# Performance work log

Measured on AMD Instinct MI355X. Metric: run time of the kernel, lower is better.

Reference implementation:

```python
import jax, jax.numpy as jnp
import numpy as np

NUM_COLORS = 10
COLOR_MAPPING_W = 0.4
CONSISTENCY_W = 0.3
RULE_W = 0.2
EXACT_BONUS = 5.0


def _color_rules(targets, num_colors):
    # Vectorized equivalent of per-batch torch.unique(): sorted unique colors
    # of each grid written into the first slots of a [B, 10] rules tensor.
    B = targets.shape[0]
    colors = jnp.arange(num_colors)
    presence = jnp.any(targets[:, :, :, None] == colors, axis=(1, 2))  # [B, 10]
    pos = jnp.cumsum(presence.astype(jnp.int32), axis=1) - 1           # slot index per color
    cols = jnp.where(presence, pos, num_colors)                        # absent -> dump slot
    rules = jnp.zeros((B, num_colors + 1), dtype=jnp.float32)
    rules = rules.at[jnp.arange(B)[:, None], cols].set(
        colors.astype(jnp.float32) * presence.astype(jnp.float32))
    return rules[:, :num_colors]


def setup_inputs() -> dict:
    key = jax.random.key(0)
    k1, k2, k3, k4 = jax.random.split(key, 4)
    B, C, H, W = 4096, NUM_COLORS, 30, 30
    return {
        "color_output": jax.random.normal(k1, (B, C, H, W), dtype=jnp.float32),
        "targets": jax.random.randint(k2, (B, H, W), 0, C),
        "color_attention": jax.random.uniform(k3, (B, H, W, C), dtype=jnp.float32),
        "lstm_rules": jax.random.normal(k4, (B, C), dtype=jnp.float32),
    }


def reference(color_output, targets, color_attention, lstm_rules):
    B, C, H, W = color_output.shape
    # exact-match cross entropy (mean over B*H*W)
    logp = jax.nn.log_softmax(color_output, axis=1)               # [B,C,H,W]
    ce = -jnp.take_along_axis(logp, targets[:, None], axis=1).mean()
    pred_colors = jnp.argmax(color_output, axis=1)                # [B,H,W]
    eq = (pred_colors == targets).astype(jnp.float32)
    exact_count = eq.sum()
    # color mapping: MSE(attention, one_hot(targets))
    onehot = jax.nn.one_hot(targets, C, dtype=jnp.float32)        # [B,H,W,C]
    color_mapping = jnp.mean((color_attention - onehot) ** 2)
    # sliding 2x2 window consistency, fused: avg over windows of (1 - mean eq)
    s = eq[:, :-1, :-1] + eq[:, 1:, :-1] + eq[:, :-1, 1:] + eq[:, 1:, 1:]
    consistency = 1.0 - s.mean() / 4.0
    # rule learning: MSE against per-batch sorted-unique-color rules
    rule_target = _color_rules(targets, C)
    rule_loss = jnp.mean((lstm_rules - rule_target) ** 2)
    total = (ce + COLOR_MAPPING_W * color_mapping
             + CONSISTENCY_W * consistency + RULE_W * rule_loss)
    total = total - (exact_count / B) * EXACT_BONUS  # bonus is 0 when count is 0
    total = jnp.maximum(total, 0.001)
    return (total, ce, color_mapping, consistency, rule_loss, exact_count)
```

## Files before the change

kernel.cpp:

```cpp
#include <hip/hip_runtime.h>


namespace {
constexpr int kB = 4096;
constexpr int kC = 10;
constexpr int kH = 30;
constexpr int kW = 30;
constexpr int kHW = kH * kW;
constexpr int kCHW = kC * kHW;
constexpr int kQuadsPerB = kHW / 4;
constexpr int kQuads = kB * kQuadsPerB;
constexpr int kAttF4 = kB * kCHW / 4;
constexpr int kGrid = 2048;
constexpr int kThreads = 256;
constexpr int kStride = kGrid * kThreads;
}

__global__ __launch_bounds__(kThreads) void iris_att_sq(
    const float* __restrict__ att_g, float* __restrict__ cmsq_part) {
    const int tid = threadIdx.x;
    float sq = 0.f;
    for (int idx = blockIdx.x * kThreads + tid; idx < kAttF4; idx += kStride) {
        const float4 v = reinterpret_cast<const float4*>(att_g)[idx];
        sq += v.x * v.x + v.y * v.y + v.z * v.z + v.w * v.w;
    }
#pragma unroll
    for (int off = 32; off > 0; off >>= 1) sq += __shfl_down(sq, off);
    __shared__ float s[4];
    if ((tid & 63) == 0) s[tid >> 6] = sq;
    __syncthreads();
    if (tid == 0) cmsq_part[blockIdx.x] = s[0] + s[1] + s[2] + s[3];
}

__global__ __launch_bounds__(kThreads) void iris_ce(
    const float* __restrict__ logits_g,
    const int* __restrict__ targets_g,
    const float* __restrict__ att_g,
    float* __restrict__ ce_part,
    float* __restrict__ cmat_part,
    unsigned* __restrict__ weq_part,
    unsigned* __restrict__ eq_part)
{
    const int tid = threadIdx.x;
    float ce_acc = 0.f, at_acc = 0.f;
    unsigned weq_acc = 0u, eq_acc = 0u;

    for (int q = blockIdx.x * kThreads + tid; q < kQuads; q += kStride) {
        const int b = q / kQuadsPerB;
        const int i = q - b * kQuadsPerB;
        const int p0 = 4 * i;

        const int4 tv = *reinterpret_cast<const int4*>(targets_g + (size_t)b * kHW + p0);
        const int ta[4] = {tv.x, tv.y, tv.z, tv.w};

        const float* __restrict__ ap = att_g + (size_t)b * kCHW + (size_t)p0 * kC;
        at_acc += ap[0 * kC + ta[0]] + ap[1 * kC + ta[1]] +
                  ap[2 * kC + ta[2]] + ap[3 * kC + ta[3]];

        const float* __restrict__ lg = logits_g + (size_t)b * kCHW + p0;
        float m[4], s[4], xt[4];
        int am[4];
#pragma unroll
        for (int j = 0; j < 4; ++j) { m[j] = -3.4e38f; s[j] = 0.f; xt[j] = 0.f; am[j] = 0; }
#pragma unroll
        for (int c = 0; c < kC; ++c) {
            const float4 v = *reinterpret_cast<const float4*>(lg + c * kHW);
            const float xv[4] = {v.x, v.y, v.z, v.w};
#pragma unroll
            for (int j = 0; j < 4; ++j) {
                const bool gt = xv[j] > m[j];
                const float mn = gt ? xv[j] : m[j];
                s[j] = s[j] * __expf(m[j] - mn) + __expf(xv[j] - mn);
                m[j] = mn;
                am[j] = gt ? c : am[j];
                xt[j] = (c == ta[j]) ? xv[j] : xt[j];
            }
        }
#pragma unroll
        for (int j = 0; j < 4; ++j) {
            ce_acc += m[j] + __logf(s[j]) - xt[j];
            const unsigned eq = (am[j] == ta[j]) ? 1u : 0u;
            eq_acc += eq;
            const int p = p0 + j;
            const int h = p / kW;
            const int w = p - h * kW;
            weq_acc += eq * (((h == 0 || h == kH - 1) ? 1u : 2u) *
                             ((w == 0 || w == kW - 1) ? 1u : 2u));
        }
    }

#pragma unroll
    for (int off = 32; off > 0; off >>= 1) {
        ce_acc  += __shfl_down(ce_acc, off);
        at_acc  += __shfl_down(at_acc, off);
        weq_acc += __shfl_down(weq_acc, off);
        eq_acc  += __shfl_down(eq_acc, off);
    }
    __shared__ float sf[2][4];
    __shared__ unsigned su[2][4];
    const int wave = tid >> 6;
    if ((tid & 63) == 0) {
        sf[0][wave] = ce_acc; sf[1][wave] = at_acc;
        su[0][wave] = weq_acc; su[1][wave] = eq_acc;
    }
    __syncthreads();
    if (tid == 0) {
        ce_part[blockIdx.x]   = sf[0][0] + sf[0][1] + sf[0][2] + sf[0][3];
        cmat_part[blockIdx.x] = sf[1][0] + sf[1][1] + sf[1][2] + sf[1][3];
        weq_part[blockIdx.x]  = su[0][0] + su[0][1] + su[0][2] + su[0][3];
        eq_part[blockIdx.x]   = su[1][0] + su[1][1] + su[1][2] + su[1][3];
    }
}

__global__ __launch_bounds__(64) void iris_rules(
    const int* __restrict__ targets_g, const float* __restrict__ rules_g,
    float* __restrict__ rule_part) {
    const int b = blockIdx.x;
    const int lane = threadIdx.x;
    const int* __restrict__ tgt = targets_g + (size_t)b * kHW;
    unsigned mask = 0u;
    for (int k = lane; k < kHW; k += 64) mask |= 1u << tgt[k];
#pragma unroll
    for (int off = 32; off > 0; off >>= 1) mask |= __shfl_down(mask, off);
    if (lane == 0) {
        const float* __restrict__ lr = rules_g + (size_t)b * kC;
        unsigned mrem = mask;
        float rl = 0.f;
#pragma unroll
        for (int s2 = 0; s2 < kC; ++s2) {
            float v = 0.f;
            if (mrem) {
                v = (float)(__ffs(mrem) - 1);
                mrem &= mrem - 1u;
            }
            const float d = lr[s2] - v;
            rl += d * d;
        }
        rule_part[b] = rl;
    }
}

__global__ __launch_bounds__(1024) void iris_finalize(
    const float* __restrict__ ce_part,
    const float* __restrict__ cmat_part,
    const float* __restrict__ cmsq_part,
    const unsigned* __restrict__ weq_part,
    const unsigned* __restrict__ eq_part,
    const float* __restrict__ rule_part,
    float* __restrict__ out) {
    const int tid = threadIdx.x;
    double ce = 0.0, cma = 0.0, cms = 0.0, rl = 0.0;
    unsigned long long weq = 0ull, eqc = 0ull;
#pragma unroll
    for (int k = 0; k < 2; ++k) {
        const int i = tid + 1024 * k;
        ce  += (double)ce_part[i];
        cma += (double)cmat_part[i];
        cms += (double)cmsq_part[i];
        weq += (unsigned long long)weq_part[i];
        eqc += (unsigned long long)eq_part[i];
    }
#pragma unroll
    for (int k = 0; k < 4; ++k) rl += (double)rule_part[tid + 1024 * k];
#pragma unroll
    for (int off = 32; off > 0; off >>= 1) {
        ce  += __shfl_down(ce, off);
        cma += __shfl_down(cma, off);
        cms += __shfl_down(cms, off);
        rl  += __shfl_down(rl, off);
        weq += __shfl_down(weq, off);
        eqc += __shfl_down(eqc, off);
    }
    __shared__ double sd[4][16];
    __shared__ unsigned long long su[2][16];
    const int wave = tid >> 6;
    if ((tid & 63) == 0) {
        sd[0][wave] = ce; sd[1][wave] = cma; sd[2][wave] = cms; sd[3][wave] = rl;
        su[0][wave] = weq; su[1][wave] = eqc;
    }
    __syncthreads();
    if (tid == 0) {
        ce = 0.0; cma = 0.0; cms = 0.0; rl = 0.0; weq = 0ull; eqc = 0ull;
#pragma unroll
        for (int i = 0; i < 16; ++i) {
            ce += sd[0][i]; cma += sd[1][i]; cms += sd[2][i]; rl += sd[3][i];
            weq += su[0][i]; eqc += su[1][i];
        }
        const double npix = (double)kB * kHW;
        const double ce_m = ce / npix;
        const double cm_m = (cms - 2.0 * cma + npix) / (npix * kC);
        const double s_mean = (double)weq / ((double)kB * (kH - 1) * (kW - 1));
        const double cons = 1.0 - s_mean / 4.0;
        const double rl_m = rl / ((double)kB * kC);
        const double exact = (double)eqc;
        double total = ce_m + 0.4 * cm_m + 0.3 * cons + 0.2 * rl_m
                       - (exact / (double)kB) * 5.0;
        if (total < 0.001) total = 0.001;
        out[0] = (float)total;
        out[1] = (float)ce_m;
        out[2] = (float)cm_m;
        out[3] = (float)cons;
        out[4] = (float)rl_m;
        out[5] = (float)exact;
    }
}

extern "C" void kernel_launch(void* const* d_in, const int* in_sizes, int n_in,
                              void* d_out, int out_size, void* d_ws, size_t ws_size,
                              hipStream_t stream) {
    const float* color_output    = (const float*)d_in[0];
    const int*   targets         = (const int*)d_in[1];
    const float* color_attention = (const float*)d_in[2];
    const float* lstm_rules      = (const float*)d_in[3];
    float* out = (float*)d_out;

    float*    ce_part   = (float*)d_ws;
    float*    cmat_part = ce_part + kGrid;
    float*    cmsq_part = cmat_part + kGrid;
    unsigned* weq_part  = (unsigned*)(cmsq_part + kGrid);
    unsigned* eq_part   = weq_part + kGrid;
    float*    rule_part = (float*)(eq_part + kGrid);

    iris_att_sq<<<kGrid, kThreads, 0, stream>>>(color_attention, cmsq_part);
    iris_ce<<<kGrid, kThreads, 0, stream>>>(color_output, targets, color_attention,
                                            ce_part, cmat_part, weq_part, eq_part);
    iris_rules<<<kB, 64, 0, stream>>>(targets, lstm_rules, rule_part);
    iris_finalize<<<1, 1024, 0, stream>>>(ce_part, cmat_part, cmsq_part,
                                          weq_part, eq_part, rule_part, out);
}
```

Measured before the change: 329.3 us.

## Fuse attention sum-of-squares pass into the cross-entropy kernel

Removes the separate attention squared-sum kernel and computes the squares inside the main kernel, which now loads each pixel quad's 40 attention values as float4 and selects the target entry from them. This avoids reading the attention tensor twice and replaces scattered gathers with contiguous loads. The grid becomes a fixed 1800 blocks with exactly two quads per thread, and the finalize loop is adapted to the new partial count. The strided per-thread float4 loads may coalesce less well, and register use rises.

```diff
diff --git a/kernel.cpp b/kernel.cpp
--- a/kernel.cpp
+++ b/kernel.cpp
@@ -10,42 +10,31 @@
 constexpr int kCHW = kC * kHW;
 constexpr int kQuadsPerB = kHW / 4;
 constexpr int kQuads = kB * kQuadsPerB;
-constexpr int kAttF4 = kB * kCHW / 4;
-constexpr int kGrid = 2048;
 constexpr int kThreads = 256;
-constexpr int kStride = kGrid * kThreads;
-}
-
-__global__ __launch_bounds__(kThreads) void iris_att_sq(
-    const float* __restrict__ att_g, float* __restrict__ cmsq_part) {
-    const int tid = threadIdx.x;
-    float sq = 0.f;
-    for (int idx = blockIdx.x * kThreads + tid; idx < kAttF4; idx += kStride) {
-        const float4 v = reinterpret_cast<const float4*>(att_g)[idx];
-        sq += v.x * v.x + v.y * v.y + v.z * v.z + v.w * v.w;
-    }
-#pragma unroll
-    for (int off = 32; off > 0; off >>= 1) sq += __shfl_down(sq, off);
-    __shared__ float s[4];
-    if ((tid & 63) == 0) s[tid >> 6] = sq;
-    __syncthreads();
-    if (tid == 0) cmsq_part[blockIdx.x] = s[0] + s[1] + s[2] + s[3];
-}
-
-__global__ __launch_bounds__(kThreads) void iris_ce(
+constexpr int kGrid = 1800;
+constexpr int kQPT = 2;
+static_assert(kGrid * kThreads * kQPT == kQuads, "work split must be exact");
+}
+
+__global__ __launch_bounds__(kThreads) void iris_fused(
     const float* __restrict__ logits_g,
     const int* __restrict__ targets_g,
     const float* __restrict__ att_g,
     float* __restrict__ ce_part,
     float* __restrict__ cmat_part,
+    float* __restrict__ cmsq_part,
     unsigned* __restrict__ weq_part,
     unsigned* __restrict__ eq_part)
 {
     const int tid = threadIdx.x;
-    float ce_acc = 0.f, at_acc = 0.f;
+    const int gid = blockIdx.x * kThreads + tid;
+
+    float ce_acc = 0.f, at_acc = 0.f, sq_acc = 0.f;
     unsigned weq_acc = 0u, eq_acc = 0u;
 
-    for (int q = blockIdx.x * kThreads + tid; q < kQuads; q += kStride) {
+#pragma unroll
+    for (int k = 0; k < kQPT; ++k) {
+        const int q = gid + k * (kGrid * kThreads);
         const int b = q / kQuadsPerB;
         const int i = q - b * kQuadsPerB;
         const int p0 = 4 * i;
@@ -54,8 +43,21 @@
         const int ta[4] = {tv.x, tv.y, tv.z, tv.w};
 
         const float* __restrict__ ap = att_g + (size_t)b * kCHW + (size_t)p0 * kC;
-        at_acc += ap[0 * kC + ta[0]] + ap[1 * kC + ta[1]] +
-                  ap[2 * kC + ta[2]] + ap[3 * kC + ta[3]];
+        float atq[4] = {0.f, 0.f, 0.f, 0.f};
+#pragma unroll
+        for (int u = 0; u < kC; ++u) {
+            const float4 v = *reinterpret_cast<const float4*>(ap + 4 * u);
+            const float av[4] = {v.x, v.y, v.z, v.w};
+#pragma unroll
+            for (int e2 = 0; e2 < 4; ++e2) {
+                const int e = 4 * u + e2;
+                const int j = e / kC;
+                const int ch = e - j * kC;
+                sq_acc += av[e2] * av[e2];
+                atq[j] = (ch == ta[j]) ? av[e2] : atq[j];
+            }
+        }
+        at_acc += atq[0] + atq[1] + atq[2] + atq[3];
 
         const float* __restrict__ lg = logits_g + (size_t)b * kCHW + p0;
         float m[4], s[4], xt[4];
@@ -93,20 +95,22 @@
     for (int off = 32; off > 0; off >>= 1) {
         ce_acc  += __shfl_down(ce_acc, off);
         at_acc  += __shfl_down(at_acc, off);
+        sq_acc  += __shfl_down(sq_acc, off);
         weq_acc += __shfl_down(weq_acc, off);
         eq_acc  += __shfl_down(eq_acc, off);
     }
-    __shared__ float sf[2][4];
+    __shared__ float sf[3][4];
     __shared__ unsigned su[2][4];
     const int wave = tid >> 6;
     if ((tid & 63) == 0) {
-        sf[0][wave] = ce_acc; sf[1][wave] = at_acc;
+        sf[0][wave] = ce_acc; sf[1][wave] = at_acc; sf[2][wave] = sq_acc;
         su[0][wave] = weq_acc; su[1][wave] = eq_acc;
     }
     __syncthreads();
     if (tid == 0) {
         ce_part[blockIdx.x]   = sf[0][0] + sf[0][1] + sf[0][2] + sf[0][3];
         cmat_part[blockIdx.x] = sf[1][0] + sf[1][1] + sf[1][2] + sf[1][3];
+        cmsq_part[blockIdx.x] = sf[2][0] + sf[2][1] + sf[2][2] + sf[2][3];
         weq_part[blockIdx.x]  = su[0][0] + su[0][1] + su[0][2] + su[0][3];
         eq_part[blockIdx.x]   = su[1][0] + su[1][1] + su[1][2] + su[1][3];
     }
@@ -151,9 +155,7 @@
     const int tid = threadIdx.x;
     double ce = 0.0, cma = 0.0, cms = 0.0, rl = 0.0;
     unsigned long long weq = 0ull, eqc = 0ull;
-#pragma unroll
-    for (int k = 0; k < 2; ++k) {
-        const int i = tid + 1024 * k;
+    for (int i = tid; i < kGrid; i += 1024) {
         ce  += (double)ce_part[i];
         cma += (double)cmat_part[i];
         cms += (double)cmsq_part[i];
@@ -221,9 +223,9 @@
     unsigned* eq_part   = weq_part + kGrid;
     float*    rule_part = (float*)(eq_part + kGrid);
 
-    iris_att_sq<<<kGrid, kThreads, 0, stream>>>(color_attention, cmsq_part);
-    iris_ce<<<kGrid, kThreads, 0, stream>>>(color_output, targets, color_attention,
-                                            ce_part, cmat_part, weq_part, eq_part);
+    iris_fused<<<kGrid, kThreads, 0, stream>>>(color_output, targets, color_attention,
+                                               ce_part, cmat_part, cmsq_part,
+                                               weq_part, eq_part);
     iris_rules<<<kB, 64, 0, stream>>>(targets, lstm_rules, rule_part);
     iris_finalize<<<1, 1024, 0, stream>>>(ce_part, cmat_part, cmsq_part,
                                           weq_part, eq_part, rule_part, out);
```

Result: slower. 341.6 us (+3.7%).
